# Kernel optimization log

Hardware: AMD Instinct MI355X
Metric: run time of the kernel (lower is better)

The kernel has to match this reference:

```python
import jax, jax.numpy as jnp
import numpy as np

REG_MAX = 16
NUM_CLASSES = 1
NUM_KPTS = 17
TOPK = 13
EPS = 1e-9

OKS_SIGMAS = np.array([0.026,0.025,0.025,0.035,0.035,0.079,0.079,0.072,0.072,0.062,0.062,0.107,0.107,0.087,0.087,0.089,0.089], np.float32)


def _bce(logits, target):
    # stable binary_cross_entropy_with_logits, reduction='none'
    return jnp.maximum(logits, 0.0) - logits * target + jnp.log1p(jnp.exp(-jnp.abs(logits)))


def _pairwise_iou(gt, pred):
    # gt [B,n,4], pred [B,L,4] -> iou [B,n,L]
    g = gt[:, :, None, :]
    p = pred[:, None, :, :]
    inter_w = jnp.clip(jnp.minimum(g[..., 2], p[..., 2]) - jnp.maximum(g[..., 0], p[..., 0]), 0.0)
    inter_h = jnp.clip(jnp.minimum(g[..., 3], p[..., 3]) - jnp.maximum(g[..., 1], p[..., 1]), 0.0)
    inter = inter_w * inter_h
    ag = (g[..., 2] - g[..., 0]) * (g[..., 3] - g[..., 1])
    ap = (p[..., 2] - p[..., 0]) * (p[..., 3] - p[..., 1])
    return inter / (ag + ap - inter + EPS)


def _assign(pred_scores_sig, pred_bboxes, anchor_points, gt_class, gt_bboxes, pad_gt_mask):
    # TaskAlignedAssigner(topk=13, alpha=1.0, beta=6.0)
    B, n, _ = gt_bboxes.shape
    L = pred_bboxes.shape[1]
    ious = _pairwise_iou(gt_bboxes, pred_bboxes)                                  # [B,n,L]
    idx = jnp.broadcast_to(gt_class, (B, n, L))
    cls = jnp.take_along_axis(jnp.swapaxes(pred_scores_sig, 1, 2), idx, axis=1)   # [B,n,L]
    metrics = cls * ious ** 6.0                                                   # alpha=1, beta=6
    ap = anchor_points[None, None, :, :]
    in_gt = ((ap[..., 0] - gt_bboxes[:, :, None, 0] > EPS)
             & (ap[..., 1] - gt_bboxes[:, :, None, 1] > EPS)
             & (gt_bboxes[:, :, None, 2] - ap[..., 0] > EPS)
             & (gt_bboxes[:, :, None, 3] - ap[..., 1] > EPS)).astype(metrics.dtype)
    _, topk_idx = jax.lax.top_k(metrics * in_gt, TOPK)                            # [B,n,K]
    topk_idx = jnp.where(pad_gt_mask > 0, topk_idx, 0)
    is_in_topk = jax.nn.one_hot(topk_idx, L, dtype=metrics.dtype).sum(-2)
    is_in_topk = jnp.where(is_in_topk > 1, 0.0, is_in_topk)
    mask_pos = is_in_topk * in_gt * pad_gt_mask                                   # [B,n,L]
    # resolve anchors assigned to multiple gts: keep gt with max iou
    is_max_iou = jnp.swapaxes(jax.nn.one_hot(ious.argmax(axis=1), n, dtype=metrics.dtype), 1, 2)
    mask_pos = jnp.where(mask_pos.sum(1, keepdims=True) > 1, is_max_iou, mask_pos)
    pos = mask_pos.sum(1) > 0                                                     # [B,L]
    assigned_gt_index = mask_pos.argmax(1)                                        # [B,L]
    bix = jnp.arange(B)[:, None]
    assigned_labels = jnp.where(pos, gt_class[bix, assigned_gt_index, 0], NUM_CLASSES)
    assigned_bboxes = gt_bboxes[bix, assigned_gt_index]                           # [B,L,4]
    one_hot_lbl = jax.nn.one_hot(assigned_labels, NUM_CLASSES + 1, dtype=metrics.dtype)[..., :NUM_CLASSES]
    # rescale alignment metrics by per-gt max iou / max metric
    m = metrics * mask_pos
    m = m / (m.max(-1, keepdims=True) + EPS) * (ious * mask_pos).max(-1, keepdims=True)
    assigned_scores = one_hot_lbl * m.max(1)[..., None]                           # [B,L,1]
    return assigned_labels, assigned_bboxes, assigned_scores, assigned_gt_index, pos


def _bbox_decode(anchor_points_s, pred_distri):
    B, L, _ = pred_distri.shape
    prob = jax.nn.softmax(pred_distri.reshape(B, L, 4, REG_MAX + 1), axis=-1)
    dist = prob @ jnp.arange(REG_MAX + 1, dtype=prob.dtype)                       # DFL projection
    return jnp.concatenate([anchor_points_s - dist[..., :2], anchor_points_s + dist[..., 2:]], -1)


def _giou(pb, gb):
    inter_w = jnp.clip(jnp.minimum(pb[..., 2], gb[..., 2]) - jnp.maximum(pb[..., 0], gb[..., 0]), 0.0)
    inter_h = jnp.clip(jnp.minimum(pb[..., 3], gb[..., 3]) - jnp.maximum(pb[..., 1], gb[..., 1]), 0.0)
    inter = inter_w * inter_h
    a1 = (pb[..., 2] - pb[..., 0]) * (pb[..., 3] - pb[..., 1])
    a2 = (gb[..., 2] - gb[..., 0]) * (gb[..., 3] - gb[..., 1])
    union = a1 + a2 - inter + EPS
    iou = inter / union
    cw = jnp.maximum(pb[..., 2], gb[..., 2]) - jnp.minimum(pb[..., 0], gb[..., 0])
    ch = jnp.maximum(pb[..., 3], gb[..., 3]) - jnp.minimum(pb[..., 1], gb[..., 1])
    area_c = cw * ch + EPS
    return 1.0 - (iou - (area_c - union) / area_c)


def _df_loss(pred_dist, target):
    # pred_dist [B,L,4,reg_max+1], target [B,L,4] in [0, reg_max-0.01]
    tl = jnp.floor(target).astype(jnp.int32)
    wl = (tl.astype(target.dtype) + 1.0) - target
    logp = jax.nn.log_softmax(pred_dist, -1)
    ll = -jnp.take_along_axis(logp, tl[..., None], -1)[..., 0]
    lr = -jnp.take_along_axis(logp, (tl + 1)[..., None], -1)[..., 0]
    return (ll * wl + lr * (1.0 - wl)).mean(-1)                                   # [B,L]


def _forward(pred_scores, pred_distri, pred_pose_logits, anchor_points, stride_tensor,
             gt_bboxes, pad_gt_mask, gt_poses, oks_sigmas, gt_class):
    B, L, _ = pred_scores.shape
    anchor_points_s = anchor_points / stride_tensor
    pred_bboxes = _bbox_decode(anchor_points_s, pred_distri)
    sgd = jax.lax.stop_gradient
    assigned_labels, assigned_bboxes, assigned_scores, assigned_gt_index, pos = _assign(
        sgd(jax.nn.sigmoid(pred_scores)), sgd(pred_bboxes * stride_tensor), anchor_points,
        gt_class, gt_bboxes, pad_gt_mask)
    assigned_bboxes = assigned_bboxes / stride_tensor
    # focal classification loss (alpha=-1 -> no alpha weighting, gamma=2)
    w = jnp.abs(jax.nn.sigmoid(pred_scores) - assigned_scores) ** 2
    ass_sum = jnp.maximum(assigned_scores.sum(), 1.0)
    loss_cls = (w * _bce(pred_scores, assigned_scores)).sum() / ass_sum
    posf = pos.astype(pred_scores.dtype)
    bbox_w = assigned_scores.sum(-1) * posf                                        # [B,L]
    loss_iou = (_giou(pred_bboxes, assigned_bboxes) * bbox_w).sum() / ass_sum
    ltrb = jnp.clip(jnp.concatenate([anchor_points_s - assigned_bboxes[..., :2],
                                     assigned_bboxes[..., 2:] - anchor_points_s], -1),
                    0.0, REG_MAX - 0.01)
    loss_dfl = (_df_loss(pred_distri.reshape(B, L, 4, REG_MAX + 1), ltrb) * bbox_w).sum() / ass_sum
    bix = jnp.arange(B)[:, None]
    kpts = gt_poses[bix, assigned_gt_index]                                        # [B,L,J,3]
    gt_xy = kpts[..., :2] / stride_tensor[None, :, None, :]
    pred_xy = pred_pose_logits[..., :2] + anchor_points_s[None, :, None, :]
    d = ((pred_xy - gt_xy) ** 2).sum(-1)                                           # [B,L,J]
    kmf = ((kpts[..., 2] != 0) & pos[..., None]).astype(d.dtype)
    area = ((assigned_bboxes[..., 2] - assigned_bboxes[..., 0])
            * (assigned_bboxes[..., 3] - assigned_bboxes[..., 1]))[..., None]
    e = d / (2.0 * oks_sigmas[None, None, :]) ** 2 / (area + EPS) / 2.0
    n_pos_kpts = jnp.maximum(posf.sum() * NUM_KPTS, 1.0)
    factor = n_pos_kpts / (kmf.sum() + EPS)
    loss_pose_reg = factor * ((1.0 - jnp.exp(-e)) * kmf).sum() / n_pos_kpts
    loss_pose_cls = (_bce(pred_pose_logits[..., 2], kmf) * posf[..., None]).sum() / n_pos_kpts
    loss = 1.0 * loss_cls + 2.5 * loss_iou + 0.5 * loss_dfl + 1.0 * loss_pose_cls + 1.0 * loss_pose_reg
    log_losses = jnp.stack([loss_cls, loss_iou, loss_dfl, loss_pose_cls, loss_pose_reg, loss])
    return loss, log_losses


def _make_anchors():
    pts, strides = [], []
    for s in (8, 16, 32):
        g = 640 // s
        xs = (np.arange(g, dtype=np.float32) + 0.5) * s
        yv, xv = np.meshgrid(xs, xs, indexing='ij')
        pts.append(np.stack([xv.ravel(), yv.ravel()], -1))
        strides.append(np.full((g * g, 1), s, np.float32))
    return jnp.asarray(np.concatenate(pts)), jnp.asarray(np.concatenate(strides))


def setup_inputs() -> dict:
    B, N, J, L = 16, 32, 17, 8400
    key = jax.random.key(0)
    ks = jax.random.split(key, 8)
    anchor_points, stride_tensor = _make_anchors()
    x1y1 = jax.random.uniform(ks[0], (B, N, 2), minval=0.0, maxval=480.0)
    wh = jax.random.uniform(ks[1], (B, N, 2), minval=32.0, maxval=160.0)
    gt_bboxes = jnp.concatenate([x1y1, x1y1 + wh], -1)
    pad_gt_mask = jnp.broadcast_to((jnp.arange(N)[None, :, None] < 24), (B, N, 1)).astype(jnp.float32)
    gt_class = jnp.zeros((B, N, 1), jnp.int32)
    ctr = x1y1 + wh / 2.0
    kxy = ctr[:, :, None, :] + jax.random.normal(ks[2], (B, N, J, 2)) * wh[:, :, None, :] * 0.2
    vis = jax.random.randint(ks[3], (B, N, J), 0, 3).astype(jnp.float32)
    gt_poses = jnp.concatenate([kxy, vis[..., None]], -1)
    pred_scores = jax.random.normal(ks[4], (B, L, 1)) * 0.5 - 2.0
    pred_distri = jax.random.normal(ks[5], (B, L, 4 * (REG_MAX + 1)))
    pred_pose_logits = jax.random.normal(ks[6], (B, L, J, 3))
    return {'pred_scores': pred_scores, 'pred_distri': pred_distri,
            'pred_pose_logits': pred_pose_logits, 'anchor_points': anchor_points,
            'stride_tensor': stride_tensor, 'gt_bboxes': gt_bboxes,
            'pad_gt_mask': pad_gt_mask, 'gt_poses': gt_poses,
            'oks_sigmas': jnp.asarray(OKS_SIGMAS), 'gt_class': gt_class}


def reference(pred_scores, pred_distri, pred_pose_logits, anchor_points, stride_tensor,
              gt_bboxes, pad_gt_mask, gt_poses, oks_sigmas, gt_class):
    return _forward(pred_scores, pred_distri, pred_pose_logits, anchor_points, stride_tensor,
                    gt_bboxes, pad_gt_mask, gt_poses, oks_sigmas, gt_class)
```

## Files before the change

### kernel.cpp

```cpp
#include <hip/hip_runtime.h>
#include <cstddef>

#define EPS 1e-9f
#define REG_MAX 16
#define TOPK 13
#define MAXL 8400
#define TPB 1024
#define CAP 1024
#define LSLOT 16

__device__ __forceinline__ float sigmoidf(float x){ return 1.0f/(1.0f+expf(-x)); }
__device__ __forceinline__ float bcef(float l, float t){
    return fmaxf(l,0.0f) - l*t + log1pf(expf(-fabsf(l)));
}
__device__ __forceinline__ float pow6f(float x){ float x2=x*x; return x2*x2*x2; }

__global__ void k_decode(const float* __restrict__ pred_scores,
                         const float* __restrict__ pred_distri,
                         const float* __restrict__ anchor_points,
                         const float* __restrict__ stride_t,
                         float* __restrict__ pred_bboxes,
                         float* __restrict__ sig,
                         unsigned int* __restrict__ words,
                         unsigned int* __restrict__ rowmax_m,
                         unsigned int* __restrict__ rowmax_i,
                         int* __restrict__ pcnt,
                         int B, int N, int L)
{
    int idx = blockIdx.x*blockDim.x + threadIdx.x;
    if (idx >= B*L) return;
    if (idx < B*N){ rowmax_m[idx]=0u; rowmax_i[idx]=0u; }
    if (idx == 0) *pcnt = 0;
    words[idx] = 0u;
    int l = idx % L;
    float v[68];
    const float4* pd4 = (const float4*)(pred_distri + (size_t)idx*68);
    #pragma unroll
    for (int i=0;i<17;i++){ float4 q = pd4[i]; v[4*i]=q.x; v[4*i+1]=q.y; v[4*i+2]=q.z; v[4*i+3]=q.w; }
    float dist[4];
    #pragma unroll
    for (int s=0;s<4;s++){
        float m = -1e30f;
        #pragma unroll
        for (int i=0;i<=REG_MAX;i++) m = fmaxf(m, v[s*17+i]);
        float sum=0.f, ws=0.f;
        #pragma unroll
        for (int i=0;i<=REG_MAX;i++){ float e = expf(v[s*17+i]-m); sum+=e; ws += e*(float)i; }
        dist[s] = ws/sum;
    }
    float st = stride_t[l];
    float ax = anchor_points[2*l]/st, ay = anchor_points[2*l+1]/st;
    float4 box = make_float4(ax-dist[0], ay-dist[1], ax+dist[2], ay+dist[3]);
    ((float4*)pred_bboxes)[idx] = box;
    sig[idx] = sigmoidf(pred_scores[idx]);
}

__global__ void k_assign_topk(const float* __restrict__ pred_bboxes,
                              const float* __restrict__ sig,
                              const float* __restrict__ anchor_points,
                              const float* __restrict__ stride_t,
                              const float* __restrict__ gt_bboxes,
                              const float* __restrict__ pad_mask,
                              float* __restrict__ ious,
                              unsigned int* __restrict__ words,
                              int B,int N,int L)
{
    __shared__ int   scnt;
    __shared__ float sval[CAP];
    __shared__ int   sidx[CAP];
    int bn = blockIdx.x; int b = bn / N; int n = bn % N;
    const float4 gb = ((const float4*)gt_bboxes)[bn];
    float gx1=gb.x, gy1=gb.y, gx2=gb.z, gy2=gb.w;
    float ag = (gx2-gx1)*(gy2-gy1);
    int tid = threadIdx.x;
    bool valid = pad_mask[bn] > 0.f;
    if (tid==0) scnt=0;
    __syncthreads();

    for (int l=tid; l<L; l+=TPB){
        float4 pb = ((const float4*)pred_bboxes)[b*L + l];
        float st = stride_t[l];
        float p0 = pb.x*st, p1 = pb.y*st, p2 = pb.z*st, p3 = pb.w*st;
        float iw = fmaxf(fminf(gx2,p2)-fmaxf(gx1,p0), 0.f);
        float ih = fmaxf(fminf(gy2,p3)-fmaxf(gy1,p1), 0.f);
        float inter = iw*ih;
        float ap = (p2-p0)*(p3-p1);
        float iou = inter/(ag+ap-inter+EPS);
        ious[(size_t)bn*L + l] = iou;
        if (valid){
            float apx = anchor_points[2*l], apy = anchor_points[2*l+1];
            bool ing = (apx-gx1>EPS)&&(apy-gy1>EPS)&&(gx2-apx>EPS)&&(gy2-apy>EPS);
            if (ing){
                float v = sig[b*L+l]*pow6f(iou);
                int slot = atomicAdd(&scnt, 1);
                if (slot < CAP){ sval[slot]=v; sidx[slot]=l; }
            }
        }
    }
    __syncthreads();
    if (!valid) return;
    int cnt = scnt < CAP ? scnt : CAP;
    unsigned int nbit = 1u<<n;

    if (cnt <= TOPK){
        for (int i=tid; i<cnt; i+=TPB)
            atomicOr(&words[b*L + sidx[i]], nbit);
        return;
    }
    if (tid >= 64) return;
    float lv[LSLOT]; int li[LSLOT];
    #pragma unroll
    for (int k=0;k<LSLOT;k++){ lv[k]=-1.f; li[k]=0x7fffffff; }
    for (int i=tid; i<cnt; i+=64){
        float cv = sval[i]; int ci = sidx[i];
        #pragma unroll
        for (int k=0;k<LSLOT;k++){
            bool better = (cv>lv[k]) || (cv==lv[k] && ci<li[k]);
            if (better){
                float tv=lv[k]; lv[k]=cv; cv=tv;
                int   ti=li[k]; li[k]=ci; ci=ti;
            }
        }
    }
    for (int r=0;r<TOPK;r++){
        float bv=lv[0]; int bl=li[0];
        #pragma unroll
        for (int off=32; off>0; off>>=1){
            float ov = __shfl_xor(bv, off);
            int   oi = __shfl_xor(bl, off);
            if (ov>bv || (ov==bv && oi<bl)){ bv=ov; bl=oi; }
        }
        if (li[0]==bl){
            atomicOr(&words[b*L + bl], nbit);
            #pragma unroll
            for (int k=0;k<LSLOT-1;k++){ lv[k]=lv[k+1]; li[k]=li[k+1]; }
            lv[LSLOT-1]=-1.f; li[LSLOT-1]=0x7fffffff;
        }
    }
}

__global__ void k_resolve(const float* __restrict__ ious,
                          const float* __restrict__ sig,
                          unsigned int* __restrict__ words,
                          unsigned int* __restrict__ rowmax_m,
                          unsigned int* __restrict__ rowmax_i,
                          int* __restrict__ poslist,
                          int* __restrict__ pcnt,
                          int B,int N,int L)
{
    int idx = blockIdx.x*blockDim.x + threadIdx.x;
    if (idx >= B*L) return;
    int b = idx / L, l = idx % L;
    unsigned int w = words[idx];
    if (!w) return;
    int n;
    if (__popc(w) > 1){
        float bv=-1e30f; int bbest=0;
        for (int nn=0;nn<N;nn++){
            float vv = ious[((size_t)(b*N+nn))*L + l];
            if (vv > bv){ bv=vv; bbest=nn; }
        }
        n = bbest;
        words[idx] = 1u<<n;
    } else {
        n = __ffs(w)-1;
    }
    float iou = ious[((size_t)(b*N+n))*L + l];
    float met = sig[idx]*pow6f(iou);
    atomicMax(&rowmax_m[b*N+n], __float_as_uint(met));
    atomicMax(&rowmax_i[b*N+n], __float_as_uint(iou));
    int slot = atomicAdd(pcnt, 1);
    poslist[slot] = idx;
}

__global__ void k_loss_all(const float* __restrict__ pred_scores,
                           const float* __restrict__ sig,
                           const float* __restrict__ ious,
                           const unsigned int* __restrict__ words,
                           const unsigned int* __restrict__ rowmax_m,
                           const unsigned int* __restrict__ rowmax_i,
                           const int* __restrict__ gt_class,
                           float* __restrict__ partials,
                           int B,int N,int L)
{
    int idx = blockIdx.x*blockDim.x + threadIdx.x;
    float a_score=0.f, a_cls=0.f;
    if (idx < B*L){
        int b=idx/L, l=idx%L;
        unsigned int w = words[idx];
        float assigned = 0.f;
        if (w){
            int n = __ffs(w)-1;
            float iou = ious[((size_t)(b*N+n))*L + l];
            float met = sig[idx]*pow6f(iou);
            float score = met/(__uint_as_float(rowmax_m[b*N+n])+EPS)
                          *__uint_as_float(rowmax_i[b*N+n]);
            if (gt_class[b*N+n]==0) assigned = score;
        }
        float logit = pred_scores[idx];
        float sg = sig[idx];
        float wg = sg - assigned; wg *= wg;
        a_cls = wg * bcef(logit, assigned);
        a_score = assigned;
    }
    #pragma unroll
    for (int off=32; off>0; off>>=1){
        a_score += __shfl_xor(a_score, off);
        a_cls   += __shfl_xor(a_cls,   off);
    }
    __shared__ float ws2[16][2];
    int wid = threadIdx.x>>6;
    if ((threadIdx.x&63)==0){ ws2[wid][0]=a_score; ws2[wid][1]=a_cls; }
    __syncthreads();
    if (threadIdx.x==0){
        float s0=0.f, s1=0.f;
        #pragma unroll
        for (int i=0;i<16;i++){ s0+=ws2[i][0]; s1+=ws2[i][1]; }
        float* row = partials + (size_t)blockIdx.x*8;
        row[0]=s0; row[1]=s1; row[2]=0.f; row[3]=0.f;
        row[4]=0.f; row[5]=0.f; row[6]=0.f; row[7]=0.f;
    }
}

__global__ void k_loss_pos(const float* __restrict__ pred_distri,
                           const float* __restrict__ pose_logits,
                           const float* __restrict__ anchor_points,
                           const float* __restrict__ stride_t,
                           const float* __restrict__ gt_bboxes,
                           const float* __restrict__ gt_poses,
                           const float* __restrict__ sigmas,
                           const int*   __restrict__ gt_class,
                           const float* __restrict__ pred_bboxes,
                           const float* __restrict__ sig,
                           const float* __restrict__ ious,
                           const unsigned int* __restrict__ words,
                           const unsigned int* __restrict__ rowmax_m,
                           const unsigned int* __restrict__ rowmax_i,
                           const int* __restrict__ poslist,
                           const int* __restrict__ pcnt,
                           float* __restrict__ partials, int rowbase,
                           int B,int N,int L,int J)
{
    int i = blockIdx.x*blockDim.x + threadIdx.x;
    int cnt = *pcnt;
    float a_giou=0,a_dfl=0,a_pos=0,a_kmf=0,a_preg=0,a_pcls=0;
    if (i < cnt){
        int idx = poslist[i];
        int b=idx/L, l=idx%L;
        int n = __ffs(words[idx])-1;
        float iou0 = ious[((size_t)(b*N+n))*L + l];
        float met = sig[idx]*pow6f(iou0);
        float score = met/(__uint_as_float(rowmax_m[b*N+n])+EPS)
                      *__uint_as_float(rowmax_i[b*N+n]);
        float assigned = (gt_class[b*N+n]==0) ? score : 0.f;
        a_pos = 1.f;
        float st = stride_t[l];
        const float4 gb4 = ((const float4*)gt_bboxes)[b*N+n];
        float ab0=gb4.x/st, ab1=gb4.y/st, ab2=gb4.z/st, ab3=gb4.w/st;
        float area = (ab2-ab0)*(ab3-ab1);
        float apx = anchor_points[2*l]/st, apy = anchor_points[2*l+1]/st;
        float bw = assigned;
        if (bw > 0.f){
            float4 pb = ((const float4*)pred_bboxes)[idx];
            float iw = fmaxf(fminf(pb.z,ab2)-fmaxf(pb.x,ab0),0.f);
            float ih = fmaxf(fminf(pb.w,ab3)-fmaxf(pb.y,ab1),0.f);
            float inter=iw*ih;
            float a1=(pb.z-pb.x)*(pb.w-pb.y);
            float a2=(ab2-ab0)*(ab3-ab1);
            float uni=a1+a2-inter+EPS;
            float iou=inter/uni;
            float cw=fmaxf(pb.z,ab2)-fminf(pb.x,ab0);
            float ch=fmaxf(pb.w,ab3)-fminf(pb.y,ab1);
            float ac=cw*ch+EPS;
            float g = 1.f-(iou-(ac-uni)/ac);
            a_giou = g*bw;
            float t4[4] = { apx-ab0, apy-ab1, ab2-apx, ab3-apy };
            const float* pdist = pred_distri + (size_t)idx*68;
            const float4* pd4 = (const float4*)pdist;
            float v[68];
            #pragma unroll
            for (int q=0;q<17;q++){ float4 qq=pd4[q]; v[4*q]=qq.x; v[4*q+1]=qq.y; v[4*q+2]=qq.z; v[4*q+3]=qq.w; }
            float dfl=0.f;
            #pragma unroll
            for (int s2=0;s2<4;s2++){
                float tt = fminf(fmaxf(t4[s2],0.f),(float)REG_MAX-0.01f);
                int tl = (int)floorf(tt);
                float wl = (float)tl + 1.f - tt;
                float m=-1e30f;
                #pragma unroll
                for (int q=0;q<=REG_MAX;q++) m=fmaxf(m,v[s2*17+q]);
                float se=0.f;
                #pragma unroll
                for (int q=0;q<=REG_MAX;q++) se+=expf(v[s2*17+q]-m);
                float lse = m + logf(se);
                float ll = -(pdist[s2*17+tl]-lse);
                float lr = -(pdist[s2*17+tl+1]-lse);
                dfl += ll*wl + lr*(1.f-wl);
            }
            a_dfl = dfl*0.25f*bw;
        }
        const float* gp = gt_poses + ((size_t)(b*N+n))*J*3;
        const float* pl = pose_logits + (size_t)idx*J*3;
        for (int j=0;j<J;j++){
            float gx=gp[3*j]/st, gy=gp[3*j+1]/st, vis=gp[3*j+2];
            float px=pl[3*j]+apx, py=pl[3*j+1]+apy, pz=pl[3*j+2];
            float kmf = (vis!=0.f)?1.f:0.f;
            float dx=px-gx, dy=py-gy;
            float d = dx*dx+dy*dy;
            float s2g = 2.f*sigmas[j]; s2g*=s2g;
            float e = d/s2g/(area+EPS)/2.f;
            a_preg += (1.f-expf(-e))*kmf;
            a_kmf  += kmf;
            a_pcls += bcef(pz, kmf);
        }
    }
    float acc[6] = {a_giou,a_dfl,a_pos,a_kmf,a_preg,a_pcls};
    #pragma unroll
    for (int k=0;k<6;k++){
        #pragma unroll
        for (int off=32; off>0; off>>=1) acc[k] += __shfl_xor(acc[k], off);
    }
    __shared__ float wsum[4][6];
    int wid = threadIdx.x>>6;
    if ((threadIdx.x&63)==0){
        #pragma unroll
        for (int k=0;k<6;k++) wsum[wid][k]=acc[k];
    }
    __syncthreads();
    if (threadIdx.x==0){
        float* row = partials + (size_t)(rowbase+blockIdx.x)*8;
        row[0]=0.f; row[1]=0.f;
        #pragma unroll
        for (int k=0;k<6;k++)
            row[2+k]=wsum[0][k]+wsum[1][k]+wsum[2][k]+wsum[3][k];
    }
}

__global__ void k_final(const float* __restrict__ partials, int nblk, int J,
                        float* __restrict__ out)
{
    __shared__ float red[256][9];
    int tid = threadIdx.x;
    float acc[8] = {0,0,0,0,0,0,0,0};
    for (int i=tid; i<nblk; i+=256){
        const float4* p = (const float4*)(partials + (size_t)i*8);
        float4 a = p[0], b = p[1];
        acc[0]+=a.x; acc[1]+=a.y; acc[2]+=a.z; acc[3]+=a.w;
        acc[4]+=b.x; acc[5]+=b.y; acc[6]+=b.z; acc[7]+=b.w;
    }
    #pragma unroll
    for (int k=0;k<8;k++) red[tid][k]=acc[k];
    __syncthreads();
    for (int s=128;s>0;s>>=1){
        if (tid<s){
            #pragma unroll
            for (int k=0;k<8;k++) red[tid][k]+=red[tid+s][k];
        }
        __syncthreads();
    }
    if (tid==0){
        float ass  = fmaxf(red[0][0],1.f);
        float lcls = red[0][1]/ass;
        float liou = red[0][2]/ass;
        float ldfl = red[0][3]/ass;
        float npk  = fmaxf(red[0][4]*(float)J,1.f);
        float factor = npk/(red[0][5]+EPS);
        float preg = factor*red[0][6]/npk;
        float pcls = red[0][7]/npk;
        float loss = lcls + 2.5f*liou + 0.5f*ldfl + pcls + preg;
        out[0]=loss; out[1]=lcls; out[2]=liou; out[3]=ldfl;
        out[4]=pcls; out[5]=preg; out[6]=loss;
    }
}

extern "C" void kernel_launch(void* const* d_in, const int* in_sizes, int n_in,
                              void* d_out, int out_size, void* d_ws, size_t ws_size,
                              hipStream_t stream)
{
    const float* pred_scores   = (const float*)d_in[0];
    const float* pred_distri   = (const float*)d_in[1];
    const float* pose_logits   = (const float*)d_in[2];
    const float* anchor_points = (const float*)d_in[3];
    const float* stride_t      = (const float*)d_in[4];
    const float* gt_bboxes     = (const float*)d_in[5];
    const float* pad_mask      = (const float*)d_in[6];
    const float* gt_poses      = (const float*)d_in[7];
    const float* sigmas        = (const float*)d_in[8];
    const int*   gt_class      = (const int*)d_in[9];

    int L = in_sizes[3]/2;
    int B = in_sizes[0]/L;
    int N = in_sizes[5]/(B*4);
    int J = in_sizes[8];

    char* ws = (char*)d_ws;
    size_t off=0;
    auto alloc=[&](size_t bytes)->void*{
        size_t cur=off; off += (bytes+255)/256*256; return (void*)(ws+cur);
    };
    float* ious           = (float*)alloc((size_t)B*N*L*4);
    float* pred_bboxes    = (float*)alloc((size_t)B*L*4*4);
    float* sig            = (float*)alloc((size_t)B*L*4);
    unsigned int* words   = (unsigned int*)alloc((size_t)B*L*4);
    unsigned int* rowmax_m= (unsigned int*)alloc((size_t)B*N*4);
    unsigned int* rowmax_i= (unsigned int*)alloc((size_t)B*N*4);
    int maxpos = B*N*TOPK;
    int* poslist          = (int*)alloc((size_t)maxpos*4);
    int* pcnt             = (int*)alloc(256);
    int nblk256  = (B*L+255)/256;
    int nblkA    = (B*L+1023)/1024;
    int nblkP    = (maxpos+255)/256;
    float* partials       = (float*)alloc((size_t)(nblkA+nblkP)*8*4);
    (void)ws_size; (void)n_in; (void)out_size;

    k_decode<<<nblk256,256,0,stream>>>(pred_scores,pred_distri,anchor_points,
                                       stride_t,pred_bboxes,sig,
                                       words,rowmax_m,rowmax_i,pcnt,B,N,L);
    k_assign_topk<<<B*N,TPB,0,stream>>>(pred_bboxes,sig,anchor_points,stride_t,
                                        gt_bboxes,pad_mask,ious,words,B,N,L);
    k_resolve<<<nblk256,256,0,stream>>>(ious,sig,words,rowmax_m,rowmax_i,
                                        poslist,pcnt,B,N,L);
    k_loss_all<<<nblkA,1024,0,stream>>>(pred_scores,sig,ious,words,
                                        rowmax_m,rowmax_i,gt_class,
                                        partials,B,N,L);
    k_loss_pos<<<nblkP,256,0,stream>>>(pred_distri,pose_logits,anchor_points,
                                       stride_t,gt_bboxes,gt_poses,sigmas,
                                       gt_class,pred_bboxes,sig,ious,words,
                                       rowmax_m,rowmax_i,poslist,pcnt,
                                       partials,nblkA,B,N,L,J);
    k_final<<<1,256,0,stream>>>(partials,nblkA+nblkP,J,(float*)d_out);
}
```

Measured before the change: 96.59 us.

## Fuse decode with per-anchor IoU over all GTs and split top-k selection

Decoding and the IoU/candidate computation are merged into one per-anchor kernel. Each thread computes IoUs against all GT boxes cached in shared memory, writes them transposed as [B,L,N], and appends in-box candidates to global per-GT lists with atomics. A separate kernel then does top-k per GT from those lists, and the dense and positive loss kernels are merged into one launch. This removes the B*N blocks that each rescan all anchors, at the cost of global atomics and candidate buffers. The hardcoded NGT=32 loop assumes N equals 32.

```diff
diff --git a/kernel.cpp b/kernel.cpp
--- a/kernel.cpp
+++ b/kernel.cpp
@@ -4,8 +4,7 @@
 #define EPS 1e-9f
 #define REG_MAX 16
 #define TOPK 13
-#define MAXL 8400
-#define TPB 1024
+#define NGT 32
 #define CAP 1024
 #define LSLOT 16
 
@@ -15,24 +14,46 @@
 }
 __device__ __forceinline__ float pow6f(float x){ float x2=x*x; return x2*x2*x2; }
 
-__global__ void k_decode(const float* __restrict__ pred_scores,
-                         const float* __restrict__ pred_distri,
-                         const float* __restrict__ anchor_points,
-                         const float* __restrict__ stride_t,
-                         float* __restrict__ pred_bboxes,
-                         float* __restrict__ sig,
-                         unsigned int* __restrict__ words,
-                         unsigned int* __restrict__ rowmax_m,
-                         unsigned int* __restrict__ rowmax_i,
-                         int* __restrict__ pcnt,
-                         int B, int N, int L)
-{
-    int idx = blockIdx.x*blockDim.x + threadIdx.x;
-    if (idx >= B*L) return;
-    if (idx < B*N){ rowmax_m[idx]=0u; rowmax_i[idx]=0u; }
-    if (idx == 0) *pcnt = 0;
+__global__ void k_zero(int* __restrict__ ccnt, unsigned int* __restrict__ rowmax_m,
+                       unsigned int* __restrict__ rowmax_i, int* __restrict__ pcnt,
+                       int BN)
+{
+    int t = threadIdx.x;
+    for (int i=t; i<BN; i+=256){ ccnt[i]=0; rowmax_m[i]=0u; rowmax_i[i]=0u; }
+    if (t==0) *pcnt = 0;
+}
+
+__global__ void k_main(const float* __restrict__ pred_scores,
+                       const float* __restrict__ pred_distri,
+                       const float* __restrict__ anchor_points,
+                       const float* __restrict__ stride_t,
+                       const float* __restrict__ gt_bboxes,
+                       const float* __restrict__ pad_mask,
+                       float* __restrict__ pred_bboxes,
+                       float* __restrict__ sig_g,
+                       float* __restrict__ ious_t,
+                       unsigned int* __restrict__ words,
+                       float2* __restrict__ cand,
+                       int* __restrict__ ccnt,
+                       int B,int N,int L,int nchunks)
+{
+    __shared__ float4 sgt[NGT];
+    __shared__ float  sag[NGT];
+    __shared__ int    sval[NGT];
+    int b = blockIdx.x / nchunks, chunk = blockIdx.x % nchunks;
+    int tid = threadIdx.x;
+    if (tid < N){
+        float4 g = ((const float4*)gt_bboxes)[b*N+tid];
+        sgt[tid] = g;
+        sag[tid] = (g.z-g.x)*(g.w-g.y);
+        sval[tid] = pad_mask[b*N+tid] > 0.f ? 1 : 0;
+    }
+    __syncthreads();
+    int l = chunk*256 + tid;
+    if (l >= L) return;
+    int idx = b*L + l;
     words[idx] = 0u;
-    int l = idx % L;
+
     float v[68];
     const float4* pd4 = (const float4*)(pred_distri + (size_t)idx*68);
     #pragma unroll
@@ -49,62 +70,49 @@
         dist[s] = ws/sum;
     }
     float st = stride_t[l];
-    float ax = anchor_points[2*l]/st, ay = anchor_points[2*l+1]/st;
+    float apx = anchor_points[2*l], apy = anchor_points[2*l+1];
+    float ax = apx/st, ay = apy/st;
     float4 box = make_float4(ax-dist[0], ay-dist[1], ax+dist[2], ay+dist[3]);
     ((float4*)pred_bboxes)[idx] = box;
-    sig[idx] = sigmoidf(pred_scores[idx]);
-}
-
-__global__ void k_assign_topk(const float* __restrict__ pred_bboxes,
-                              const float* __restrict__ sig,
-                              const float* __restrict__ anchor_points,
-                              const float* __restrict__ stride_t,
-                              const float* __restrict__ gt_bboxes,
-                              const float* __restrict__ pad_mask,
-                              float* __restrict__ ious,
-                              unsigned int* __restrict__ words,
-                              int B,int N,int L)
-{
-    __shared__ int   scnt;
-    __shared__ float sval[CAP];
-    __shared__ int   sidx[CAP];
-    int bn = blockIdx.x; int b = bn / N; int n = bn % N;
-    const float4 gb = ((const float4*)gt_bboxes)[bn];
-    float gx1=gb.x, gy1=gb.y, gx2=gb.z, gy2=gb.w;
-    float ag = (gx2-gx1)*(gy2-gy1);
+    float sg = sigmoidf(pred_scores[idx]);
+    sig_g[idx] = sg;
+
+    float p0 = box.x*st, p1 = box.y*st, p2 = box.z*st, p3 = box.w*st;
+    float ap_area = (p2-p0)*(p3-p1);
+    float row[NGT];
+    #pragma unroll
+    for (int n=0;n<NGT;n++){
+        float4 g = sgt[n];
+        float iw = fmaxf(fminf(g.z,p2)-fmaxf(g.x,p0), 0.f);
+        float ih = fmaxf(fminf(g.w,p3)-fmaxf(g.y,p1), 0.f);
+        float inter = iw*ih;
+        float iou = inter/(sag[n]+ap_area-inter+EPS);
+        row[n] = iou;
+        bool ing = (apx-g.x>EPS)&&(apy-g.y>EPS)&&(g.z-apx>EPS)&&(g.w-apy>EPS);
+        if (ing && sval[n]){
+            float mv = sg*pow6f(iou);
+            int slot = atomicAdd(&ccnt[b*N+n], 1);
+            if (slot < CAP) cand[(size_t)(b*N+n)*CAP+slot] = make_float2(mv, __int_as_float(l));
+        }
+    }
+    float4* dst = (float4*)(ious_t + (size_t)idx*N);
+    #pragma unroll
+    for (int q=0;q<NGT/4;q++)
+        dst[q] = make_float4(row[4*q],row[4*q+1],row[4*q+2],row[4*q+3]);
+}
+
+__global__ void k_select(const float2* __restrict__ cand,
+                         const int* __restrict__ ccnt,
+                         unsigned int* __restrict__ words,
+                         int B,int N,int L)
+{
+    int bn = blockIdx.x; int b = bn/N, n = bn%N;
+    int cnt = ccnt[bn]; cnt = cnt < CAP ? cnt : CAP;
     int tid = threadIdx.x;
-    bool valid = pad_mask[bn] > 0.f;
-    if (tid==0) scnt=0;
-    __syncthreads();
-
-    for (int l=tid; l<L; l+=TPB){
-        float4 pb = ((const float4*)pred_bboxes)[b*L + l];
-        float st = stride_t[l];
-        float p0 = pb.x*st, p1 = pb.y*st, p2 = pb.z*st, p3 = pb.w*st;
-        float iw = fmaxf(fminf(gx2,p2)-fmaxf(gx1,p0), 0.f);
-        float ih = fmaxf(fminf(gy2,p3)-fmaxf(gy1,p1), 0.f);
-        float inter = iw*ih;
-        float ap = (p2-p0)*(p3-p1);
-        float iou = inter/(ag+ap-inter+EPS);
-        ious[(size_t)bn*L + l] = iou;
-        if (valid){
-            float apx = anchor_points[2*l], apy = anchor_points[2*l+1];
-            bool ing = (apx-gx1>EPS)&&(apy-gy1>EPS)&&(gx2-apx>EPS)&&(gy2-apy>EPS);
-            if (ing){
-                float v = sig[b*L+l]*pow6f(iou);
-                int slot = atomicAdd(&scnt, 1);
-                if (slot < CAP){ sval[slot]=v; sidx[slot]=l; }
-            }
-        }
-    }
-    __syncthreads();
-    if (!valid) return;
-    int cnt = scnt < CAP ? scnt : CAP;
     unsigned int nbit = 1u<<n;
-
+    const float2* my = cand + (size_t)bn*CAP;
     if (cnt <= TOPK){
-        for (int i=tid; i<cnt; i+=TPB)
-            atomicOr(&words[b*L + sidx[i]], nbit);
+        if (tid < cnt) atomicOr(&words[b*L + __float_as_int(my[tid].y)], nbit);
         return;
     }
     if (tid >= 64) return;
@@ -112,7 +120,8 @@
     #pragma unroll
     for (int k=0;k<LSLOT;k++){ lv[k]=-1.f; li[k]=0x7fffffff; }
     for (int i=tid; i<cnt; i+=64){
-        float cv = sval[i]; int ci = sidx[i];
+        float2 e = my[i];
+        float cv = e.x; int ci = __float_as_int(e.y);
         #pragma unroll
         for (int k=0;k<LSLOT;k++){
             bool better = (cv>lv[k]) || (cv==lv[k] && ci<li[k]);
@@ -139,7 +148,7 @@
     }
 }
 
-__global__ void k_resolve(const float* __restrict__ ious,
+__global__ void k_resolve(const float* __restrict__ ious_t,
                           const float* __restrict__ sig,
                           unsigned int* __restrict__ words,
                           unsigned int* __restrict__ rowmax_m,
@@ -150,14 +159,16 @@
 {
     int idx = blockIdx.x*blockDim.x + threadIdx.x;
     if (idx >= B*L) return;
-    int b = idx / L, l = idx % L;
+    int b = idx / L;
     unsigned int w = words[idx];
     if (!w) return;
+    const float* irow = ious_t + (size_t)idx*N;
     int n;
     if (__popc(w) > 1){
         float bv=-1e30f; int bbest=0;
-        for (int nn=0;nn<N;nn++){
-            float vv = ious[((size_t)(b*N+nn))*L + l];
+        #pragma unroll
+        for (int nn=0;nn<NGT;nn++){
+            float vv = irow[nn];
             if (vv > bv){ bv=vv; bbest=nn; }
         }
         n = bbest;
@@ -165,7 +176,7 @@
     } else {
         n = __ffs(w)-1;
     }
-    float iou = ious[((size_t)(b*N+n))*L + l];
+    float iou = irow[n];
     float met = sig[idx]*pow6f(iou);
     atomicMax(&rowmax_m[b*N+n], __float_as_uint(met));
     atomicMax(&rowmax_i[b*N+n], __float_as_uint(iou));
@@ -173,25 +184,37 @@
     poslist[slot] = idx;
 }
 
-__global__ void k_loss_all(const float* __restrict__ pred_scores,
-                           const float* __restrict__ sig,
-                           const float* __restrict__ ious,
-                           const unsigned int* __restrict__ words,
-                           const unsigned int* __restrict__ rowmax_m,
-                           const unsigned int* __restrict__ rowmax_i,
-                           const int* __restrict__ gt_class,
-                           float* __restrict__ partials,
-                           int B,int N,int L)
-{
-    int idx = blockIdx.x*blockDim.x + threadIdx.x;
-    float a_score=0.f, a_cls=0.f;
+__global__ void k_loss(const float* __restrict__ pred_scores,
+                       const float* __restrict__ pred_distri,
+                       const float* __restrict__ pose_logits,
+                       const float* __restrict__ anchor_points,
+                       const float* __restrict__ stride_t,
+                       const float* __restrict__ gt_bboxes,
+                       const float* __restrict__ gt_poses,
+                       const float* __restrict__ sigmas,
+                       const int*   __restrict__ gt_class,
+                       const float* __restrict__ pred_bboxes,
+                       const float* __restrict__ sig,
+                       const float* __restrict__ ious_t,
+                       const unsigned int* __restrict__ words,
+                       const unsigned int* __restrict__ rowmax_m,
+                       const unsigned int* __restrict__ rowmax_i,
+                       const int* __restrict__ poslist,
+                       const int* __restrict__ pcnt,
+                       float* __restrict__ partials,
+                       int B,int N,int L,int J)
+{
+    int tid = threadIdx.x;
+    float a_score=0,a_cls=0,a_giou=0,a_dfl=0,a_pos=0,a_kmf=0,a_preg=0,a_pcls=0;
+
+    int idx = blockIdx.x*blockDim.x + tid;
     if (idx < B*L){
-        int b=idx/L, l=idx%L;
+        int b = idx/L;
         unsigned int w = words[idx];
         float assigned = 0.f;
         if (w){
             int n = __ffs(w)-1;
-            float iou = ious[((size_t)(b*N+n))*L + l];
+            float iou = ious_t[(size_t)idx*N + n];
             float met = sig[idx]*pow6f(iou);
             float score = met/(__uint_as_float(rowmax_m[b*N+n])+EPS)
                           *__uint_as_float(rowmax_i[b*N+n]);
@@ -203,53 +226,15 @@
         a_cls = wg * bcef(logit, assigned);
         a_score = assigned;
     }
-    #pragma unroll
-    for (int off=32; off>0; off>>=1){
-        a_score += __shfl_xor(a_score, off);
-        a_cls   += __shfl_xor(a_cls,   off);
-    }
-    __shared__ float ws2[16][2];
-    int wid = threadIdx.x>>6;
-    if ((threadIdx.x&63)==0){ ws2[wid][0]=a_score; ws2[wid][1]=a_cls; }
-    __syncthreads();
-    if (threadIdx.x==0){
-        float s0=0.f, s1=0.f;
-        #pragma unroll
-        for (int i=0;i<16;i++){ s0+=ws2[i][0]; s1+=ws2[i][1]; }
-        float* row = partials + (size_t)blockIdx.x*8;
-        row[0]=s0; row[1]=s1; row[2]=0.f; row[3]=0.f;
-        row[4]=0.f; row[5]=0.f; row[6]=0.f; row[7]=0.f;
-    }
-}
-
-__global__ void k_loss_pos(const float* __restrict__ pred_distri,
-                           const float* __restrict__ pose_logits,
-                           const float* __restrict__ anchor_points,
-                           const float* __restrict__ stride_t,
-                           const float* __restrict__ gt_bboxes,
-                           const float* __restrict__ gt_poses,
-                           const float* __restrict__ sigmas,
-                           const int*   __restrict__ gt_class,
-                           const float* __restrict__ pred_bboxes,
-                           const float* __restrict__ sig,
-                           const float* __restrict__ ious,
-                           const unsigned int* __restrict__ words,
-                           const unsigned int* __restrict__ rowmax_m,
-                           const unsigned int* __restrict__ rowmax_i,
-                           const int* __restrict__ poslist,
-                           const int* __restrict__ pcnt,
-                           float* __restrict__ partials, int rowbase,
-                           int B,int N,int L,int J)
-{
-    int i = blockIdx.x*blockDim.x + threadIdx.x;
+
     int cnt = *pcnt;
-    float a_giou=0,a_dfl=0,a_pos=0,a_kmf=0,a_preg=0,a_pcls=0;
-    if (i < cnt){
-        int idx = poslist[i];
-        int b=idx/L, l=idx%L;
-        int n = __ffs(words[idx])-1;
-        float iou0 = ious[((size_t)(b*N+n))*L + l];
-        float met = sig[idx]*pow6f(iou0);
+    int e = blockIdx.x + tid*gridDim.x;
+    if (e < cnt){
+        int pidx = poslist[e];
+        int b = pidx/L, l = pidx%L;
+        int n = __ffs(words[pidx])-1;
+        float iou0 = ious_t[(size_t)pidx*N + n];
+        float met = sig[pidx]*pow6f(iou0);
         float score = met/(__uint_as_float(rowmax_m[b*N+n])+EPS)
                       *__uint_as_float(rowmax_i[b*N+n]);
         float assigned = (gt_class[b*N+n]==0) ? score : 0.f;
@@ -261,7 +246,7 @@
         float apx = anchor_points[2*l]/st, apy = anchor_points[2*l+1]/st;
         float bw = assigned;
         if (bw > 0.f){
-            float4 pb = ((const float4*)pred_bboxes)[idx];
+            float4 pb = ((const float4*)pred_bboxes)[pidx];
             float iw = fmaxf(fminf(pb.z,ab2)-fmaxf(pb.x,ab0),0.f);
             float ih = fmaxf(fminf(pb.w,ab3)-fmaxf(pb.y,ab1),0.f);
             float inter=iw*ih;
@@ -275,7 +260,7 @@
             float g = 1.f-(iou-(ac-uni)/ac);
             a_giou = g*bw;
             float t4[4] = { apx-ab0, apy-ab1, ab2-apx, ab3-apy };
-            const float* pdist = pred_distri + (size_t)idx*68;
+            const float* pdist = pred_distri + (size_t)pidx*68;
             const float4* pd4 = (const float4*)pdist;
             float v[68];
             #pragma unroll
@@ -300,7 +285,7 @@
             a_dfl = dfl*0.25f*bw;
         }
         const float* gp = gt_poses + ((size_t)(b*N+n))*J*3;
-        const float* pl = pose_logits + (size_t)idx*J*3;
+        const float* pl = pose_logits + (size_t)pidx*J*3;
         for (int j=0;j<J;j++){
             float gx=gp[3*j]/st, gy=gp[3*j+1]/st, vis=gp[3*j+2];
             float px=pl[3*j]+apx, py=pl[3*j+1]+apy, pz=pl[3*j+2];
@@ -308,31 +293,31 @@
             float dx=px-gx, dy=py-gy;
             float d = dx*dx+dy*dy;
             float s2g = 2.f*sigmas[j]; s2g*=s2g;
-            float e = d/s2g/(area+EPS)/2.f;
-            a_preg += (1.f-expf(-e))*kmf;
+            float ee = d/s2g/(area+EPS)/2.f;
+            a_preg += (1.f-expf(-ee))*kmf;
             a_kmf  += kmf;
             a_pcls += bcef(pz, kmf);
         }
     }
-    float acc[6] = {a_giou,a_dfl,a_pos,a_kmf,a_preg,a_pcls};
-    #pragma unroll
-    for (int k=0;k<6;k++){
+
+    float acc[8] = {a_score,a_cls,a_giou,a_dfl,a_pos,a_kmf,a_preg,a_pcls};
+    #pragma unroll
+    for (int k=0;k<8;k++){
         #pragma unroll
         for (int off=32; off>0; off>>=1) acc[k] += __shfl_xor(acc[k], off);
     }
-    __shared__ float wsum[4][6];
-    int wid = threadIdx.x>>6;
-    if ((threadIdx.x&63)==0){
-        #pragma unroll
-        for (int k=0;k<6;k++) wsum[wid][k]=acc[k];
+    __shared__ float wsum[8][8];
+    int wid = tid>>6;
+    if ((tid&63)==0){
+        #pragma unroll
+        for (int k=0;k<8;k++) wsum[wid][k]=acc[k];
     }
     __syncthreads();
-    if (threadIdx.x==0){
-        float* row = partials + (size_t)(rowbase+blockIdx.x)*8;
-        row[0]=0.f; row[1]=0.f;
-        #pragma unroll
-        for (int k=0;k<6;k++)
-            row[2+k]=wsum[0][k]+wsum[1][k]+wsum[2][k]+wsum[3][k];
+    if (tid<8){
+        float s=0.f;
+        #pragma unroll
+        for (int i=0;i<8;i++) s += wsum[i][tid];
+        partials[(size_t)blockIdx.x*8+tid]=s;
     }
 }
 
@@ -398,35 +383,35 @@
     auto alloc=[&](size_t bytes)->void*{
         size_t cur=off; off += (bytes+255)/256*256; return (void*)(ws+cur);
     };
-    float* ious           = (float*)alloc((size_t)B*N*L*4);
+    float* ious_t         = (float*)alloc((size_t)B*L*N*4);
     float* pred_bboxes    = (float*)alloc((size_t)B*L*4*4);
     float* sig            = (float*)alloc((size_t)B*L*4);
     unsigned int* words   = (unsigned int*)alloc((size_t)B*L*4);
     unsigned int* rowmax_m= (unsigned int*)alloc((size_t)B*N*4);
     unsigned int* rowmax_i= (unsigned int*)alloc((size_t)B*N*4);
+    float2* cand          = (float2*)alloc((size_t)B*N*CAP*8);
+    int* ccnt             = (int*)alloc((size_t)B*N*4);
     int maxpos = B*N*TOPK;
     int* poslist          = (int*)alloc((size_t)maxpos*4);
     int* pcnt             = (int*)alloc(256);
-    int nblk256  = (B*L+255)/256;
-    int nblkA    = (B*L+1023)/1024;
-    int nblkP    = (maxpos+255)/256;
-    float* partials       = (float*)alloc((size_t)(nblkA+nblkP)*8*4);
+    int nchunks  = (L+255)/256;
+    int nblkR    = (B*L+255)/256;
+    int nblkL    = (B*L+511)/512;
+    float* partials       = (float*)alloc((size_t)nblkL*8*4);
     (void)ws_size; (void)n_in; (void)out_size;
 
-    k_decode<<<nblk256,256,0,stream>>>(pred_scores,pred_distri,anchor_points,
-                                       stride_t,pred_bboxes,sig,
-                                       words,rowmax_m,rowmax_i,pcnt,B,N,L);
-    k_assign_topk<<<B*N,TPB,0,stream>>>(pred_bboxes,sig,anchor_points,stride_t,
-                                        gt_bboxes,pad_mask,ious,words,B,N,L);
-    k_resolve<<<nblk256,256,0,stream>>>(ious,sig,words,rowmax_m,rowmax_i,
-                                        poslist,pcnt,B,N,L);
-    k_loss_all<<<nblkA,1024,0,stream>>>(pred_scores,sig,ious,words,
-                                        rowmax_m,rowmax_i,gt_class,
-                                        partials,B,N,L);
-    k_loss_pos<<<nblkP,256,0,stream>>>(pred_distri,pose_logits,anchor_points,
-                                       stride_t,gt_bboxes,gt_poses,sigmas,
-                                       gt_class,pred_bboxes,sig,ious,words,
-                                       rowmax_m,rowmax_i,poslist,pcnt,
-                                       partials,nblkA,B,N,L,J);
-    k_final<<<1,256,0,stream>>>(partials,nblkA+nblkP,J,(float*)d_out);
-}
+    k_zero<<<1,256,0,stream>>>(ccnt,rowmax_m,rowmax_i,pcnt,B*N);
+    k_main<<<B*nchunks,256,0,stream>>>(pred_scores,pred_distri,anchor_points,
+                                       stride_t,gt_bboxes,pad_mask,
+                                       pred_bboxes,sig,ious_t,words,cand,ccnt,
+                                       B,N,L,nchunks);
+    k_select<<<B*N,256,0,stream>>>(cand,ccnt,words,B,N,L);
+    k_resolve<<<nblkR,256,0,stream>>>(ious_t,sig,words,rowmax_m,rowmax_i,
+                                      poslist,pcnt,B,N,L);
+    k_loss<<<nblkL,512,0,stream>>>(pred_scores,pred_distri,pose_logits,
+                                   anchor_points,stride_t,gt_bboxes,gt_poses,
+                                   sigmas,gt_class,pred_bboxes,sig,ious_t,
+                                   words,rowmax_m,rowmax_i,poslist,pcnt,
+                                   partials,B,N,L,J);
+    k_final<<<1,256,0,stream>>>(partials,nblkL,J,(float*)d_out);
+}
```

New measurement: 99.17 us. 1.03x slower.
